# Performance work log

Hardware: AMD Instinct MI355X
Metric: run time of the kernel (lower is better)

## Reference

```python
import jax, jax.numpy as jnp
import numpy as np

NEG_INF = -1e30

def _pool_unpool(x, k):
    # x: [B, C, H, W]. Non-overlapping max pool with window k (floor-mode,
    # matching torch MaxPool2d default), then MaxUnpool: scatter the pooled max
    # back to its argmax location within each window, zeros elsewhere.
    B, C, H, W = x.shape
    Hc, Wc = (H // k) * k, (W // k) * k  # cropped region covered by windows
    xc = x[:, :, :Hc, :Wc]
    # reshape into windows: [B, C, H/k, k, W/k, k] -> [B, C, H/k, W/k, k*k]
    xw = xc.reshape(B, C, Hc // k, k, Wc // k, k).transpose(0, 1, 2, 4, 3, 5)
    xw = xw.reshape(B, C, Hc // k, Wc // k, k * k)
    mx = jnp.max(xw, axis=-1, keepdims=True)
    am = jnp.argmax(xw, axis=-1)  # first max index, matches torch tie-breaking
    onehot = (jnp.arange(k * k) == am[..., None])
    yw = jnp.where(onehot, mx, jnp.zeros_like(mx))
    yc = yw.reshape(B, C, Hc // k, Wc // k, k, k).transpose(0, 1, 2, 4, 3, 5)
    yc = yc.reshape(B, C, Hc, Wc)
    # output_size=size in torch unpool -> pad uncovered border with zeros
    return jnp.pad(yc, ((0, 0), (0, 0), (0, H - Hc), (0, W - Wc)))

def setup_inputs() -> dict:
    key = jax.random.key(0)
    x = jax.random.uniform(key, (16, 1, 1080, 1920), dtype=jnp.float32)
    return {"x": x}

def reference(x):
    k = 3
    x = _pool_unpool(x, k)
    x = _pool_unpool(x, k + 2)
    x = _pool_unpool(x, k + 3)
    return x
```

## Files before the change

### kernel.cpp

```cpp
#include <hip/hip_runtime.h>
#include <stdint.h>


#define IMG_H 1080
#define IMG_W 1920
#define TILE_H 30
#define TILE_W 240
#define NTHREADS 256
#define V4PR (TILE_W / 4)
#define NV4 (TILE_H * V4PR)

#define NSX (IMG_W / TILE_W)
#define NSY (IMG_H / TILE_H)
#define NB 16
#define NSTRIPS (NSX * NSY * NB)
#define NBLOCKS 512
#define SPB (NSTRIPS / NBLOCKS)

#define GPTR(p) ((const __attribute__((address_space(1))) void*)(p))
#define LPTR(p) ((__attribute__((address_space(3))) void*)(p))

template <int K>
__device__ __forceinline__ void nms_stage(float (*tile)[TILE_W], int t) {
    constexpr int NWR = TILE_H / K;
    constexpr int NWC = TILE_W / K;
    for (int w = t; w < NWR * NWC; w += NTHREADS) {
        const int wr = w / NWC;
        const int wc = w - wr * NWC;
        const int r0 = wr * K;
        const int c0 = wc * K;
        float mx = -1.0f;
        int am = 0;
#pragma unroll
        for (int r = 0; r < K; ++r)
#pragma unroll
            for (int c = 0; c < K; ++c) {
                const float v = tile[r0 + r][c0 + c];
                if (v > mx) { mx = v; am = r * K + c; }
            }
#pragma unroll
        for (int r = 0; r < K; ++r)
#pragma unroll
            for (int c = 0; c < K; ++c)
                tile[r0 + r][c0 + c] = (r * K + c == am) ? mx : 0.0f;
    }
}

__global__ __launch_bounds__(NTHREADS) void pooling_nms_kernel(
    const float* __restrict__ x, float* __restrict__ out) {
    __shared__ float tile[2][TILE_H][TILE_W];

    const int t = threadIdx.x;
    const int s0 = blockIdx.x * SPB;

    const int r_t = t / V4PR;
    const int c4_t = t - r_t * V4PR;

    auto strip_base = [&](int s) -> size_t {
        const int xs = s % NSX;
        const int rem = s / NSX;
        const int ys = rem % NSY;
        const int z = rem / NSY;
        return (size_t)z * (IMG_H * (size_t)IMG_W) +
               (size_t)(ys * TILE_H) * IMG_W + (size_t)xs * TILE_W;
    };

    auto prefetch = [&](int s, int buf) {
        const float* src = x + strip_base(s);
        int r = r_t, c4 = c4_t;
        for (int v = t; v < NV4; v += NTHREADS) {
            __builtin_amdgcn_global_load_lds(
                GPTR(src + (size_t)r * IMG_W + c4 * 4),
                LPTR((char*)&tile[buf][0][0] + (size_t)v * 16), 16, 0, 0);
            r += 4; c4 += 16;
            if (c4 >= V4PR) { c4 -= V4PR; r += 1; }
        }
    };

    auto store_strip = [&](int s, int buf) {
        float* dst = out + strip_base(s);
        int r = r_t, c4 = c4_t;
        for (int v = t; v < NV4; v += NTHREADS) {
            *reinterpret_cast<float4*>(dst + (size_t)r * IMG_W + c4 * 4) =
                *reinterpret_cast<const float4*>(&tile[buf][r][c4 * 4]);
            r += 4; c4 += 16;
            if (c4 >= V4PR) { c4 -= V4PR; r += 1; }
        }
    };

    prefetch(s0, 0);
    asm volatile("s_waitcnt vmcnt(0)\n\ts_barrier" ::: "memory");

    for (int i = 0; i < SPB; ++i) {
        const int buf = i & 1;
        if (i + 1 < SPB) prefetch(s0 + i + 1, buf ^ 1);

        nms_stage<3>(tile[buf], t);
        asm volatile("s_waitcnt lgkmcnt(0)\n\ts_barrier" ::: "memory");
        nms_stage<5>(tile[buf], t);
        asm volatile("s_waitcnt lgkmcnt(0)\n\ts_barrier" ::: "memory");
        nms_stage<6>(tile[buf], t);
        asm volatile("s_waitcnt lgkmcnt(0)\n\ts_barrier" ::: "memory");

        store_strip(s0 + i, buf);
        asm volatile("s_waitcnt vmcnt(7) lgkmcnt(0)\n\ts_barrier" ::: "memory");
    }
}

extern "C" void kernel_launch(void* const* d_in, const int* in_sizes, int n_in,
                              void* d_out, int out_size, void* d_ws, size_t ws_size,
                              hipStream_t stream) {
    const float* x = (const float*)d_in[0];
    float* out = (float*)d_out;
    pooling_nms_kernel<<<dim3(NBLOCKS), NTHREADS, 0, stream>>>(x, out);
}
```

Before: 249.6 us.

## Keep strip segments in registers and do separable row/column pooling

Each thread now loads a 30-element row segment of the tile into registers and runs all three pooling stages there. Each stage computes per-row horizontal maxima, exchanges them through a small padded LDS buffer, reduces vertically to find the winning row, and zeroes non-winners locally. The output is staged back through the reused LDS buffer for coalesced stores, and the double-buffered input tile is replaced by a single tile plus the horizontal-max buffers. This cuts the repeated shared-memory traffic of the per-window loops, at the cost of more barriers per stage and only 240 of the 256 threads doing the pooling.

```diff
diff --git a/kernel.cpp b/kernel.cpp
--- a/kernel.cpp
+++ b/kernel.cpp
@@ -12,49 +12,90 @@
 
 #define NSX (IMG_W / TILE_W)
 #define NSY (IMG_H / TILE_H)
-#define NB 16
-#define NSTRIPS (NSX * NSY * NB)
+#define NBI 16
+#define NSTRIPS (NSX * NSY * NBI)
 #define NBLOCKS 512
 #define SPB (NSTRIPS / NBLOCKS)
 
+#define HSTRIDE 132
+#define HREG (TILE_H * HSTRIDE)
+
 #define GPTR(p) ((const __attribute__((address_space(1))) void*)(p))
 #define LPTR(p) ((__attribute__((address_space(3))) void*)(p))
+#define BAR_LGKM() asm volatile("s_waitcnt lgkmcnt(0)\n\ts_barrier" ::: "memory")
+#define BAR_VM0()  asm volatile("s_waitcnt vmcnt(0) lgkmcnt(0)\n\ts_barrier" ::: "memory")
+#define BAR_VM7()  asm volatile("s_waitcnt vmcnt(7) lgkmcnt(0)\n\ts_barrier" ::: "memory")
 
 template <int K>
-__device__ __forceinline__ void nms_stage(float (*tile)[TILE_W], int t) {
-    constexpr int NWR = TILE_H / K;
-    constexpr int NWC = TILE_W / K;
-    for (int w = t; w < NWR * NWC; w += NTHREADS) {
-        const int wr = w / NWC;
-        const int wc = w - wr * NWC;
-        const int r0 = wr * K;
-        const int c0 = wc * K;
-        float mx = -1.0f;
-        int am = 0;
+__device__ __forceinline__ void stage(float (&v)[TILE_H], float* __restrict__ hreg,
+                                      int r, int sseg, bool act) {
+    constexpr int NH = TILE_H / K;
+    constexpr int NG = (NH + 3) / 4;
+    if (act) {
+        float hpad[NG * 4];
 #pragma unroll
-        for (int r = 0; r < K; ++r)
+        for (int q = 0; q < NG * 4; ++q) hpad[q] = 0.0f;
+#pragma unroll
+        for (int j = 0; j < NH; ++j) {
+            float m = v[j * K];
+#pragma unroll
+            for (int c = 1; c < K; ++c) m = fmaxf(m, v[j * K + c]);
+            hpad[j] = m;
+        }
+        float* hp = hreg + r * HSTRIDE + sseg * 16;
+#pragma unroll
+        for (int q = 0; q < NG; ++q)
+            *reinterpret_cast<float4*>(hp + 4 * q) =
+                *reinterpret_cast<const float4*>(&hpad[4 * q]);
+    }
+    BAR_LGKM();
+    if (act) {
+        const int g = r / K;
+        const int myrr = r - g * K;
+        float best[NH];
+        int frow[NH];
+#pragma unroll
+        for (int j = 0; j < NH; ++j) { best[j] = -1.0f; frow[j] = -1; }
+        const float* vb = hreg + (g * K) * HSTRIDE + sseg * 16;
+#pragma unroll
+        for (int rr = 0; rr < K; ++rr) {
+            float hr[NG * 4];
+#pragma unroll
+            for (int q = 0; q < NG; ++q)
+                *reinterpret_cast<float4*>(&hr[4 * q]) =
+                    *reinterpret_cast<const float4*>(vb + rr * HSTRIDE + 4 * q);
+#pragma unroll
+            for (int j = 0; j < NH; ++j)
+                if (hr[j] > best[j]) { best[j] = hr[j]; frow[j] = rr; }
+        }
+#pragma unroll
+        for (int j = 0; j < NH; ++j) {
+            const bool rowwin = (frow[j] == myrr);
+            bool seen = false;
 #pragma unroll
             for (int c = 0; c < K; ++c) {
-                const float v = tile[r0 + r][c0 + c];
-                if (v > mx) { mx = v; am = r * K + c; }
+                const int idx = j * K + c;
+                const bool eq = (v[idx] == best[j]);
+                if (!(rowwin && eq && !seen)) v[idx] = 0.0f;
+                seen = seen || eq;
             }
-#pragma unroll
-        for (int r = 0; r < K; ++r)
-#pragma unroll
-            for (int c = 0; c < K; ++c)
-                tile[r0 + r][c0 + c] = (r * K + c == am) ? mx : 0.0f;
+        }
     }
 }
 
 __global__ __launch_bounds__(NTHREADS) void pooling_nms_kernel(
     const float* __restrict__ x, float* __restrict__ out) {
-    __shared__ float tile[2][TILE_H][TILE_W];
+    __shared__ float tile[TILE_H * TILE_W];
+    __shared__ float bbuf[2 * HREG];
 
     const int t = threadIdx.x;
     const int s0 = blockIdx.x * SPB;
+    const bool act = t < TILE_H * 8;
+    const int r = t >> 3;
+    const int sseg = t & 7;
 
-    const int r_t = t / V4PR;
-    const int c4_t = t - r_t * V4PR;
+    const int rv = t / V4PR;
+    const int cv = t - rv * V4PR;
 
     auto strip_base = [&](int s) -> size_t {
         const int xs = s % NSX;
@@ -65,45 +106,59 @@
                (size_t)(ys * TILE_H) * IMG_W + (size_t)xs * TILE_W;
     };
 
-    auto prefetch = [&](int s, int buf) {
+    auto prefetch = [&](int s) {
         const float* src = x + strip_base(s);
-        int r = r_t, c4 = c4_t;
-        for (int v = t; v < NV4; v += NTHREADS) {
+        int rr = rv, cc = cv;
+        for (int vv = t; vv < NV4; vv += NTHREADS) {
             __builtin_amdgcn_global_load_lds(
-                GPTR(src + (size_t)r * IMG_W + c4 * 4),
-                LPTR((char*)&tile[buf][0][0] + (size_t)v * 16), 16, 0, 0);
-            r += 4; c4 += 16;
-            if (c4 >= V4PR) { c4 -= V4PR; r += 1; }
+                GPTR(src + (size_t)rr * IMG_W + cc * 4),
+                LPTR((char*)tile + (size_t)vv * 16), 16, 0, 0);
+            rr += 4; cc += 16;
+            if (cc >= V4PR) { cc -= V4PR; rr += 1; }
         }
     };
 
-    auto store_strip = [&](int s, int buf) {
-        float* dst = out + strip_base(s);
-        int r = r_t, c4 = c4_t;
-        for (int v = t; v < NV4; v += NTHREADS) {
-            *reinterpret_cast<float4*>(dst + (size_t)r * IMG_W + c4 * 4) =
-                *reinterpret_cast<const float4*>(&tile[buf][r][c4 * 4]);
-            r += 4; c4 += 16;
-            if (c4 >= V4PR) { c4 -= V4PR; r += 1; }
-        }
-    };
+    float v[TILE_H];
 
-    prefetch(s0, 0);
-    asm volatile("s_waitcnt vmcnt(0)\n\ts_barrier" ::: "memory");
+    prefetch(s0);
+    BAR_VM0();
 
     for (int i = 0; i < SPB; ++i) {
-        const int buf = i & 1;
-        if (i + 1 < SPB) prefetch(s0 + i + 1, buf ^ 1);
+        if (act) {
+            const float* tp = &tile[r * TILE_W + sseg * 30];
+#pragma unroll
+            for (int k = 0; k < 15; ++k)
+                *reinterpret_cast<float2*>(&v[2 * k]) =
+                    *reinterpret_cast<const float2*>(&tp[2 * k]);
+        }
+        BAR_LGKM();
+        if (i + 1 < SPB) prefetch(s0 + i + 1);
 
-        nms_stage<3>(tile[buf], t);
-        asm volatile("s_waitcnt lgkmcnt(0)\n\ts_barrier" ::: "memory");
-        nms_stage<5>(tile[buf], t);
-        asm volatile("s_waitcnt lgkmcnt(0)\n\ts_barrier" ::: "memory");
-        nms_stage<6>(tile[buf], t);
-        asm volatile("s_waitcnt lgkmcnt(0)\n\ts_barrier" ::: "memory");
+        stage<3>(v, bbuf, r, sseg, act);
+        stage<5>(v, bbuf + HREG, r, sseg, act);
+        stage<6>(v, bbuf, r, sseg, act);
 
-        store_strip(s0 + i, buf);
-        asm volatile("s_waitcnt vmcnt(7) lgkmcnt(0)\n\ts_barrier" ::: "memory");
+        BAR_LGKM();
+        if (act) {
+            float* bp = &bbuf[r * TILE_W + sseg * 30];
+#pragma unroll
+            for (int k = 0; k < 15; ++k)
+                *reinterpret_cast<float2*>(&bp[2 * k]) =
+                    *reinterpret_cast<const float2*>(&v[2 * k]);
+        }
+        BAR_LGKM();
+
+        {
+            float* dst = out + strip_base(s0 + i);
+            int rr = rv, cc = cv;
+            for (int vv = t; vv < NV4; vv += NTHREADS) {
+                *reinterpret_cast<float4*>(dst + (size_t)rr * IMG_W + cc * 4) =
+                    *reinterpret_cast<const float4*>(&bbuf[vv * 4]);
+                rr += 4; cc += 16;
+                if (cc >= V4PR) { cc -= V4PR; rr += 1; }
+            }
+        }
+        BAR_VM7();
     }
 }
 
```

Result: no change. 249.7 us (+0.1%).
